# Optimization experiments

Measured on AMD Instinct MI355X. Metric: run time of the kernel, lower is better.

The kernel has to match this reference:

```python
import jax, jax.numpy as jnp
import numpy as np
from jax import lax

B, S = 64, 256            # batch, max_seq_len
EMB = 1024                # embed (== decoder_hidden, required by outs buffer)
ENC = 512                 # encoder_hidden; 2*ENC = 1024
DEC = 1024                # decoder_hidden
GIN = EMB + 2 * ENC       # GRUCell input size = 2048


def setup_inputs() -> dict:
    key = jax.random.key(0)
    ks = jax.random.split(key, 12)
    w = 0.02
    inp = {
        "input": jax.random.normal(ks[0], (B, S, EMB), jnp.float32),
        "hidden": jax.random.normal(ks[1], (DEC, B), jnp.float32),  # [decoder_hidden, batch]
        "encoder_outs": jax.random.normal(ks[2], (B, S, 2 * ENC), jnp.float32),
        "lengths": jnp.maximum(jax.random.randint(ks[3], (B,), 0, S), 1).astype(jnp.int32),
        # Attention params (additive / Bahdanau): v^T tanh(W_enc*enc + W_dec*h)
        "W_enc": jax.random.normal(ks[4], (2 * ENC, DEC), jnp.float32) * w,
        "W_dec": jax.random.normal(ks[5], (DEC, DEC), jnp.float32) * w,
        "v": jax.random.normal(ks[6], (DEC,), jnp.float32) * w,
        # GRUCell params (torch layout: W_ih [3H, GIN], W_hh [3H, H])
        "W_ih": jax.random.normal(ks[7], (3 * DEC, GIN), jnp.float32) * w,
        "W_hh": jax.random.normal(ks[8], (3 * DEC, DEC), jnp.float32) * w,
        "b_ih": jax.random.normal(ks[9], (3 * DEC,), jnp.float32) * w,
        "b_hh": jax.random.normal(ks[10], (3 * DEC,), jnp.float32) * w,
    }
    return inp


def reference(input, hidden, encoder_outs, lengths, W_enc, W_dec, v, W_ih, W_hh, b_ih, b_hh):
    h0 = hidden.T                                  # [B, DEC]
    mask = jnp.arange(S)[None, :] < lengths[:, None]   # [B, S]
    enc_proj = encoder_outs @ W_enc                # [B, S, DEC] (hoisted out of the loop)

    # One shared teacher-forcing coin flip per timestep (torch.rand(1) < 0.5),
    # made deterministic with a fixed key.
    tf_flags = jax.random.uniform(jax.random.key(1), (S - 1,)) < 0.5

    def attention(h):
        # energy: [B, S]
        energy = jnp.tanh(enc_proj + (h @ W_dec)[:, None, :]) @ v
        energy = jnp.where(mask, energy, jnp.float32(-1e9))
        attn = jax.nn.softmax(energy, axis=1)
        return jnp.einsum("bs,bse->be", attn, encoder_outs)  # [B, 2*ENC]

    def gru_cell(x, h):
        gi = x @ W_ih.T + b_ih                     # [B, 3*DEC]
        gh = h @ W_hh.T + b_hh
        i_r, i_z, i_n = jnp.split(gi, 3, axis=1)
        h_r, h_z, h_n = jnp.split(gh, 3, axis=1)
        r = jax.nn.sigmoid(i_r + h_r)
        z = jax.nn.sigmoid(i_z + h_z)
        n = jnp.tanh(i_n + r * h_n)
        return (1.0 - z) * n + z * h

    # teacher inputs for step t are input[:, t-1, :], t = 1..S-1
    teach_seq = jnp.swapaxes(input, 0, 1)[: S - 1]  # [S-1, B, EMB]

    def step(carry, xt):
        h, prev = carry
        teach, tf = xt
        ctx = attention(h)
        sel = jnp.where(tf, teach, prev)            # scalar bool broadcast
        h_new = gru_cell(jnp.concatenate([sel, ctx], axis=1), h)
        return (h_new, h_new), h_new

    (_, _), hs = lax.scan(step, (h0, input[:, 0, :]), (teach_seq, tf_flags))
    outs = jnp.concatenate([input[:, 0:1, :], jnp.swapaxes(hs, 0, 1)], axis=1)  # [B, S, DEC]
    return outs
```

## Files before the change

### kernel.cpp

```cpp
#include <hip/hip_runtime.h>
#include <stdint.h>

typedef unsigned short u16;
typedef unsigned int   u32;
typedef unsigned long long u64;
typedef __attribute__((ext_vector_type(8))) short short8;
typedef __attribute__((ext_vector_type(4))) short s16x4;
typedef __attribute__((ext_vector_type(4))) float f32x4;

#define MFMA(a,b,c) __builtin_amdgcn_mfma_f32_16x16x32_bf16((a),(b),(c),0,0,0)
#define NBLK 256
#define NTHR 256
#define SMEM_BYTES 160832

static const long kOutB = 256*1024;

__device__ __forceinline__ float b2f(u16 v){ union{u32 u; float f;} c; c.u = ((u32)v)<<16; return c.f; }
__device__ __forceinline__ u16 f2b(float f){ union{float f; u32 u;} c; c.f = f; u32 r = c.u + 0x7FFFu + ((c.u>>16)&1u); return (u16)(r>>16); }
__device__ __forceinline__ float fexp2(float x){ return __builtin_amdgcn_exp2f(x); }
__device__ __forceinline__ float frcp(float x){ return __builtin_amdgcn_rcpf(x); }
__device__ __forceinline__ float tanh_(float x){ float e = fexp2(x*2.885390081777927f); return 1.f - 2.f*frcp(e+1.f); }
__device__ __forceinline__ float sigm_(float x){ return frcp(1.f + fexp2(-1.4426950408889634f*x)); }

__device__ __forceinline__ u64 ald64(const void* p){
    return __hip_atomic_load((const u64*)p, __ATOMIC_RELAXED, __HIP_MEMORY_SCOPE_AGENT);
}
__device__ __forceinline__ u32 ald32(const void* p){
    return __hip_atomic_load((const u32*)p, __ATOMIC_RELAXED, __HIP_MEMORY_SCOPE_AGENT);
}
__device__ __forceinline__ void ast64(void* p, u64 v){
    __hip_atomic_store((u64*)p, v, __ATOMIC_RELAXED, __HIP_MEMORY_SCOPE_AGENT);
}
__device__ __forceinline__ void ast32(void* p, u32 v){
    __hip_atomic_store((u32*)p, v, __ATOMIC_RELAXED, __HIP_MEMORY_SCOPE_AGENT);
}

__device__ __forceinline__ u32 rotl32_(u32 x, int r){ return (x << r) | (x >> (32 - r)); }
__device__ bool tf_bit(u32 j){
    const u32 k0 = 0u, k1 = 1u, k2 = 0x1BD11BDAu ^ 0u ^ 1u;
    const int R0[4] = {13,15,26,6}, R1[4] = {17,29,16,24};
    u32 x0 = 0u, x1 = j;
    x0 += k0; x1 += k1;
    for(int i=0;i<4;i++){ x0 += x1; x1 = rotl32_(x1,R0[i]); x1 ^= x0; }
    x0 += k1; x1 += k2 + 1u;
    for(int i=0;i<4;i++){ x0 += x1; x1 = rotl32_(x1,R1[i]); x1 ^= x0; }
    x0 += k2; x1 += k0 + 2u;
    for(int i=0;i<4;i++){ x0 += x1; x1 = rotl32_(x1,R0[i]); x1 ^= x0; }
    x0 += k0; x1 += k1 + 3u;
    for(int i=0;i<4;i++){ x0 += x1; x1 = rotl32_(x1,R1[i]); x1 ^= x0; }
    x0 += k1; x1 += k2 + 4u;
    for(int i=0;i<4;i++){ x0 += x1; x1 = rotl32_(x1,R0[i]); x1 ^= x0; }
    x0 += k2; x1 += k0 + 5u;
    return (((x0 ^ x1) >> 31) == 0u);
}

__device__ __forceinline__ void gridbar(u32* sync){
    asm volatile("s_waitcnt vmcnt(0)" ::: "memory");
    __syncthreads();
    if(threadIdx.x == 0){
        u32* cnt  = sync;
        u32* gen  = sync + 32;
        u32* gcnt = sync + 64 + (blockIdx.x >> 5)*32;
        u32 g = __hip_atomic_load(gen, __ATOMIC_RELAXED, __HIP_MEMORY_SCOPE_AGENT);
        u32 a = __hip_atomic_fetch_add(gcnt, 1u, __ATOMIC_RELAXED, __HIP_MEMORY_SCOPE_AGENT);
        bool done = false;
        if(a == 31u){
            __hip_atomic_store(gcnt, 0u, __ATOMIC_RELAXED, __HIP_MEMORY_SCOPE_AGENT);
            asm volatile("s_waitcnt vmcnt(0)" ::: "memory");
            u32 b = __hip_atomic_fetch_add(cnt, 1u, __ATOMIC_RELAXED, __HIP_MEMORY_SCOPE_AGENT);
            if(b == 7u){
                __hip_atomic_store(cnt, 0u, __ATOMIC_RELAXED, __HIP_MEMORY_SCOPE_AGENT);
                asm volatile("s_waitcnt vmcnt(0)" ::: "memory");
                __hip_atomic_store(gen, g + 1u, __ATOMIC_RELAXED, __HIP_MEMORY_SCOPE_AGENT);
                done = true;
            }
        }
        if(!done)
            while(__hip_atomic_load(gen, __ATOMIC_RELAXED, __HIP_MEMORY_SCOPE_AGENT) == g)
                __builtin_amdgcn_s_sleep(1);
    }
    __syncthreads();
}

__global__ void k_cvt(const float* __restrict__ in, u16* __restrict__ out, int n){
    int i = blockIdx.x*blockDim.x + threadIdx.x;
    int st = gridDim.x*blockDim.x;
    for(; i < n; i += st) out[i] = f2b(in[i]);
}

__global__ void k_cvt_t(const float* __restrict__ in, u16* __restrict__ out, int R, int C){
    __shared__ float tile[32][33];
    int bx = blockIdx.x, by = blockIdx.y;
    int tx = threadIdx.x, ty = threadIdx.y;
    for(int j = 0; j < 32; j += 8) tile[ty+j][tx] = in[(by*32+ty+j)*C + bx*32+tx];
    __syncthreads();
    for(int j = 0; j < 32; j += 8) out[(bx*32+ty+j)*R + by*32+tx] = f2b(tile[tx][ty+j]);
}

__global__ void k_init(const float* __restrict__ hidden, const float* __restrict__ input,
                       float* __restrict__ h0f, u16* __restrict__ h0b, float* __restrict__ out,
                       u32* __restrict__ sync){
    int i = blockIdx.x*blockDim.x + threadIdx.x;
    int b = i >> 10, d = i & 1023;
    float h = hidden[d*64 + b];
    h0f[i] = h; h0b[i] = f2b(h);
    out[(long)b*kOutB + d] = input[(long)b*kOutB + d];
    if(i < 512) sync[i] = 0u;
}

__global__ __launch_bounds__(256) void k_gemm_ep(const u16* __restrict__ A, const u16* __restrict__ BT,
                                                 u16* __restrict__ Cb){
    int m0 = blockIdx.x*64, n0 = blockIdx.y*64;
    int w = threadIdx.x >> 6, l = threadIdx.x & 63;
    int r0 = l & 15, kh = (l >> 4) * 8;
    const u16* arow = A + (long)(m0 + w*16 + r0)*1024 + kh;
    f32x4 acc[4] = {};
    for(int k0 = 0; k0 < 1024; k0 += 32){
        short8 a = *(const short8*)(arow + k0);
        #pragma unroll
        for(int j = 0; j < 4; ++j){
            short8 b = *(const short8*)(BT + (long)(n0 + j*16 + r0)*1024 + k0 + kh);
            acc[j] = MFMA(a, b, acc[j]);
        }
    }
    int orow = m0 + w*16 + (l>>4)*4;
    int ocol = n0 + (l & 15);
    #pragma unroll
    for(int j = 0; j < 4; ++j)
        #pragma unroll
        for(int r = 0; r < 4; ++r)
            Cb[(long)(orow + r)*1024 + ocol + j*16] = f2b(acc[j][r]);
}

__global__ __launch_bounds__(NTHR, 1) void k_steps(
        const u16* __restrict__ epb, const float* __restrict__ input, const u16* __restrict__ encb,
        const u16* __restrict__ wihb, const u16* __restrict__ whhb, const u16* __restrict__ wdecT,
        const float* __restrict__ bih, const float* __restrict__ bhh,
        const float* __restrict__ vv, const int* __restrict__ lengths,
        float* __restrict__ hWrot, long hWstride,
        float* __restrict__ enyrot, long enystride,
        u16* __restrict__ crot, const float* __restrict__ hf0, u16* __restrict__ hrot,
        float* __restrict__ out, u32* __restrict__ sync){
    extern __shared__ char smem[];
    u16*   s_ep = (u16*)smem;
    float* sB   = (float*)(smem + 131072);
    float* sA   = (float*)(smem + 135168);
    float* sRed = (float*)(smem + 136192);
    f32x4* sAcc = (f32x4*)(smem + 136256);

    const int bid = blockIdx.x, tid = threadIdx.x;
    const int w = tid >> 6, l = tid & 63;
    const int r0 = l & 15, kh = (l >> 4) * 8;
    const int rg = bid >> 6, cg = bid & 63;
    const int p2_b = bid >> 2, p2_sq = bid & 3;
    const bool rotOn = (hWstride != 0);

    const int p2_len = lengths[p2_b];
    float rv[16];
    #pragma unroll
    for(int j = 0; j < 16; ++j) rv[j] = vv[l*16 + j];

    {
        const u16* src = epb + (long)(p2_b*256 + p2_sq*64)*1024;
        for(int i = tid; i < 8192; i += NTHR)
            *(short8*)(s_ep + i*8) = *(const short8*)(src + i*8);
    }
    __syncthreads();

    const u16* p1_brow = wdecT + (long)(cg*16 + r0)*1024 + w*256 + kh;
    const long p1_aoff = (long)(rg*16 + r0)*1024 + w*256 + kh;
    const int kxb = w*512, khb = w*256;
    const u16* b_wr = wihb + (long)(       cg*16 + r0)*2048 + kxb + kh;
    const u16* b_wz = wihb + (long)(1024 + cg*16 + r0)*2048 + kxb + kh;
    const u16* b_wn = wihb + (long)(2048 + cg*16 + r0)*2048 + kxb + kh;
    const u16* b_vr = whhb + (long)(       cg*16 + r0)*1024 + khb + kh;
    const u16* b_vz = whhb + (long)(1024 + cg*16 + r0)*1024 + khb + kh;
    const u16* b_vn = whhb + (long)(2048 + cg*16 + r0)*1024 + khb + kh;
    const long a_row_off = (long)(rg*16 + r0)*1024;
    const float* g_inf = input + (long)(rg*16 + r0)*kOutB;
    const int ucol = cg*16 + (l & 15);
    const float bir = bih[ucol], biz = bih[1024+ucol], bin_ = bih[2048+ucol];
    const float bhr = bhh[ucol], bhz = bhh[1024+ucol], bhn = bhh[2048+ucol];
    const int erow = rg*16 + (l>>4)*4;
    float hold[4];
    #pragma unroll
    for(int r = 0; r < 4; ++r) hold[r] = hf0[(erow + r)*1024 + ucol];

    for(int t = 1; t < 256; ++t){
        const u16* hbo = hrot + (size_t)(t-1)*65536;
        u16*       hbn = hrot + (size_t)t*65536;
        u16*       ctxt = crot + (size_t)(t-1)*65536;
        float*     hWt  = hWrot  + (size_t)(t-1)*hWstride;
        float*     enyt = enyrot + (size_t)(t-1)*enystride;
        {
            const u16* arow = hbo + p1_aoff;
            f32x4 acc = {};
            #pragma unroll
            for(int k0 = 0; k0 < 256; k0 += 32)
                acc = MFMA(*(const short8*)(arow + k0), *(const short8*)(p1_brow + k0), acc);
            sAcc[w*64 + l] = acc;
            __syncthreads();
            if(w == 0){
                f32x4 s = sAcc[l];
                s += sAcc[64 + l]; s += sAcc[128 + l]; s += sAcc[192 + l];
                #pragma unroll
                for(int r = 0; r < 4; ++r){
                    float mine = s[r];
                    float oth = __shfl_xor(mine, 1);
                    if(!(l & 1)){
                        union{ float f[2]; u64 q; } pk; pk.f[0] = mine; pk.f[1] = oth;
                        ast64(hWt + (erow + r)*1024 + cg*16 + (l & 15), pk.q);
                    }
                }
            }
        }
        gridbar(sync);
        {
            float rh[16];
            const float* hp = hWt + p2_b*1024 + l*16;
            if(rotOn){
                #pragma unroll
                for(int j4 = 0; j4 < 4; ++j4){
                    f32x4 v4 = *(const f32x4*)(hp + j4*4);
                    rh[j4*4+0] = v4.x; rh[j4*4+1] = v4.y;
                    rh[j4*4+2] = v4.z; rh[j4*4+3] = v4.w;
                }
            } else {
                #pragma unroll
                for(int j = 0; j < 8; ++j){
                    union{ u64 q; float f[2]; } uu; uu.q = ald64(hp + j*2);
                    rh[2*j] = uu.f[0]; rh[2*j+1] = uu.f[1];
                }
            }
            const u16* lrow = s_ep + (w*16)*1024 + l*16;
            for(int si = 0; si < 16; ++si){
                int s = p2_sq*64 + w*16 + si;
                short8 q0 = *(const short8*)(lrow + si*1024);
                short8 q1 = *(const short8*)(lrow + si*1024 + 8);
                float acc = 0.f;
                #pragma unroll
                for(int j = 0; j < 8; ++j) acc += rv[j]   * tanh_(b2f((u16)q0[j]) + rh[j]);
                #pragma unroll
                for(int j = 0; j < 8; ++j) acc += rv[8+j] * tanh_(b2f((u16)q1[j]) + rh[8+j]);
                #pragma unroll
                for(int off = 32; off; off >>= 1) acc += __shfl_xor(acc, off);
                if(l == 0){
                    float val = (s < p2_len) ? acc : -1e9f;
                    ast32(enyt + p2_b*256 + s, __float_as_uint(val));
                }
            }
        }
        gridbar(sync);
        {
            float e = rotOn ? enyt[p2_b*256 + tid]
                            : __uint_as_float(ald32(enyt + p2_b*256 + tid));
            float m = e;
            #pragma unroll
            for(int off = 32; off; off >>= 1) m = fmaxf(m, __shfl_xor(m, off));
            if(l == 0) sRed[w] = m;
            __syncthreads();
            m = fmaxf(fmaxf(sRed[0], sRed[1]), fmaxf(sRed[2], sRed[3]));
            float pp = fexp2((e - m)*1.4426950408889634f);
            sA[tid] = pp;
            float sm = pp;
            #pragma unroll
            for(int off = 32; off; off >>= 1) sm += __shfl_xor(sm, off);
            if(l == 0) sRed[4 + w] = sm;
            __syncthreads();
            float inv = 1.f / (sRed[4] + sRed[5] + sRed[6] + sRed[7]);
            const int half = l >> 5, cl = l & 31;
            const u16* ebase = encb + (long)p2_b*262144 + p2_sq*256 + cl*8;
            float acc[8] = {};
            #pragma unroll 8
            for(int i = 0; i < 32; ++i){
                int s = w*64 + i*2 + half;
                float ps = sA[s];
                short8 q = *(const short8*)(ebase + (long)s*1024);
                #pragma unroll
                for(int j = 0; j < 8; ++j) acc[j] += ps*b2f((u16)q[j]);
            }
            #pragma unroll
            for(int j = 0; j < 8; ++j) acc[j] += __shfl_xor(acc[j], 32);
            if(half == 0){
                #pragma unroll
                for(int j = 0; j < 8; ++j) sB[w*256 + cl*8 + j] = acc[j];
            }
            __syncthreads();
            float c = (sB[tid] + sB[256+tid] + sB[512+tid] + sB[768+tid]) * inv;
            u32 cb = (u32)f2b(c);
            u32 ob = (u32)__shfl_xor((int)cb, 1);
            if(!(tid & 1))
                ast32((u32*)ctxt + ((p2_b*1024 + p2_sq*256 + tid) >> 1), cb | (ob << 16));
        }
        gridbar(sync);
        {
            const bool useTeach = (t == 1) || tf_bit((u32)(t - 1));
            f32x4 a_r = {}, a_z = {}, a_n = {};
            if(w < 2){
                if(useTeach){
                    const float* sf = g_inf + (long)(t - 1)*1024 + kxb + kh;
                    for(int k0 = 0; k0 < 512; k0 += 32){
                        f32x4 u0q = *(const f32x4*)(sf + k0);
                        f32x4 u1q = *(const f32x4*)(sf + k0 + 4);
                        short8 a;
                        a[0]=(short)f2b(u0q.x); a[1]=(short)f2b(u0q.y);
                        a[2]=(short)f2b(u0q.z); a[3]=(short)f2b(u0q.w);
                        a[4]=(short)f2b(u1q.x); a[5]=(short)f2b(u1q.y);
                        a[6]=(short)f2b(u1q.z); a[7]=(short)f2b(u1q.w);
                        a_r = MFMA(a, *(const short8*)(b_wr + k0), a_r);
                        a_z = MFMA(a, *(const short8*)(b_wz + k0), a_z);
                        a_n = MFMA(a, *(const short8*)(b_wn + k0), a_n);
                    }
                } else {
                    const u16* ar = hbo + a_row_off + kxb + kh;
                    for(int k0 = 0; k0 < 512; k0 += 32){
                        short8 a = *(const short8*)(ar + k0);
                        a_r = MFMA(a, *(const short8*)(b_wr + k0), a_r);
                        a_z = MFMA(a, *(const short8*)(b_wz + k0), a_z);
                        a_n = MFMA(a, *(const short8*)(b_wn + k0), a_n);
                    }
                }
            } else {
                const u16* ar = ctxt + a_row_off + (kxb - 1024) + kh;
                for(int k0 = 0; k0 < 512; k0 += 32){
                    short8 a = *(const short8*)(ar + k0);
                    a_r = MFMA(a, *(const short8*)(b_wr + k0), a_r);
                    a_z = MFMA(a, *(const short8*)(b_wz + k0), a_z);
                    a_n = MFMA(a, *(const short8*)(b_wn + k0), a_n);
                }
            }
            f32x4 h_r = {}, h_z = {}, h_n = {};
            {
                const u16* ah = hbo + a_row_off + khb + kh;
                #pragma unroll
                for(int k0 = 0; k0 < 256; k0 += 32){
                    short8 h = *(const short8*)(ah + k0);
                    h_r = MFMA(h, *(const short8*)(b_vr + k0), h_r);
                    h_z = MFMA(h, *(const short8*)(b_vz + k0), h_z);
                    h_n = MFMA(h, *(const short8*)(b_vn + k0), h_n);
                }
            }
            sAcc[(w*6+0)*64 + l] = a_r;
            sAcc[(w*6+1)*64 + l] = a_z;
            sAcc[(w*6+2)*64 + l] = a_n;
            sAcc[(w*6+3)*64 + l] = h_r;
            sAcc[(w*6+4)*64 + l] = h_z;
            sAcc[(w*6+5)*64 + l] = h_n;
            __syncthreads();
            if(w == 0){
                f32x4 air = sAcc[0*64+l] + sAcc[6*64+l] + sAcc[12*64+l] + sAcc[18*64+l];
                f32x4 aiz = sAcc[1*64+l] + sAcc[7*64+l] + sAcc[13*64+l] + sAcc[19*64+l];
                f32x4 ain = sAcc[2*64+l] + sAcc[8*64+l] + sAcc[14*64+l] + sAcc[20*64+l];
                f32x4 ahr = sAcc[3*64+l] + sAcc[9*64+l] + sAcc[15*64+l] + sAcc[21*64+l];
                f32x4 ahz = sAcc[4*64+l] + sAcc[10*64+l] + sAcc[16*64+l] + sAcc[22*64+l];
                f32x4 ahn = sAcc[5*64+l] + sAcc[11*64+l] + sAcc[17*64+l] + sAcc[23*64+l];
                #pragma unroll
                for(int r = 0; r < 4; ++r){
                    int b = erow + r;
                    float rgt = sigm_(air[r] + bir + ahr[r] + bhr);
                    float z   = sigm_(aiz[r] + biz + ahz[r] + bhz);
                    float n   = tanh_(ain[r] + bin_ + rgt*(ahn[r] + bhn));
                    float hn = (1.f - z)*n + z*hold[r];
                    hold[r] = hn;
                    out[(long)b*kOutB + (long)t*1024 + ucol] = hn;
                    u32 mb = (u32)f2b(hn);
                    u32 ob = (u32)__shfl_xor((int)mb, 1);
                    if(!(l & 1))
                        ast32((u32*)hbn + ((b*1024 + ucol) >> 1), mb | (ob << 16));
                }
            }
        }
        gridbar(sync);
    }
}

extern "C" void kernel_launch(void* const* d_in, const int* in_sizes, int n_in,
                              void* d_out, int out_size, void* d_ws, size_t ws_size,
                              hipStream_t stream){
    (void)in_sizes; (void)n_in; (void)out_size;
    const float* input    = (const float*)d_in[0];
    const float* hidden   = (const float*)d_in[1];
    const float* enc_outs = (const float*)d_in[2];
    const int*   lengths  = (const int*)  d_in[3];
    const float* W_enc    = (const float*)d_in[4];
    const float* W_dec    = (const float*)d_in[5];
    const float* v        = (const float*)d_in[6];
    const float* W_ih     = (const float*)d_in[7];
    const float* W_hh     = (const float*)d_in[8];
    const float* b_ih     = (const float*)d_in[9];
    const float* b_hh     = (const float*)d_in[10];
    float* out = (float*)d_out;

    char* p = (char*)d_ws;
    auto alloc = [&](size_t bytes){ void* r = (void*)p; p += (bytes + 255) & ~(size_t)255; return r; };
    u16* epb   = (u16*)alloc((size_t)16384*1024*2);
    u16* encb  = (u16*)alloc((size_t)16384*1024*2);
    u16* wihb  = (u16*)alloc((size_t)3072*2048*2);
    u16* whhb  = (u16*)alloc((size_t)3072*1024*2);
    u16* wencT = (u16*)alloc((size_t)1024*1024*2);
    u16* wdecT = (u16*)alloc((size_t)1024*1024*2);
    float* hf0 = (float*)alloc((size_t)64*1024*4);
    u16* hrot  = (u16*)alloc((size_t)256*65536*2);
    u16* crot  = (u16*)alloc((size_t)255*65536*2);
    u32* sync  = (u32*)alloc(2048);
    size_t used = (size_t)(p - (char*)d_ws);
    size_t rotBytes = ((size_t)255*65536*4 + 256) + ((size_t)255*16384*4 + 256);
    long hWstride, enystride;
    float *hWrot, *enyrot;
    if(used + rotBytes <= ws_size){
        hWrot  = (float*)alloc((size_t)255*65536*4);
        enyrot = (float*)alloc((size_t)255*16384*4);
        hWstride = 65536; enystride = 16384;
    } else {
        hWrot  = (float*)alloc((size_t)65536*4);
        enyrot = (float*)alloc((size_t)16384*4);
        hWstride = 0; enystride = 0;
    }
    if((size_t)(p - (char*)d_ws) > ws_size) return;

    k_cvt<<<2048, 256, 0, stream>>>(enc_outs, encb, 16384*1024);
    k_cvt<<<1024, 256, 0, stream>>>(W_ih,     wihb, 3072*2048);
    k_cvt<<<512,  256, 0, stream>>>(W_hh,     whhb, 3072*1024);
    k_cvt_t<<<dim3(32,32), dim3(32,8), 0, stream>>>(W_enc, wencT, 1024, 1024);
    k_cvt_t<<<dim3(32,32), dim3(32,8), 0, stream>>>(W_dec, wdecT, 1024, 1024);
    k_init<<<256, 256, 0, stream>>>(hidden, input, hf0, hrot, out, sync);
    k_gemm_ep<<<dim3(256,16), 256, 0, stream>>>(encb, wencT, epb);

    hipFuncSetAttribute((const void*)k_steps, hipFuncAttributeMaxDynamicSharedMemorySize, SMEM_BYTES);
    k_steps<<<NBLK, NTHR, SMEM_BYTES, stream>>>(epb, input, encb, wihb, whhb, wdecT,
                                                b_ih, b_hh, v, lengths,
                                                hWrot, hWstride, enyrot, enystride,
                                                crot, hf0, hrot,
                                                out, sync);
}
```

Baseline: 10.25 ms.

## Replace grid barriers with per-group dataflow flags and store hW in bf16

```diff
diff --git a/kernel.cpp b/kernel.cpp
--- a/kernel.cpp
+++ b/kernel.cpp
@@ -82,6 +82,20 @@
     __syncthreads();
 }
 
+__device__ __forceinline__ void flag_signal(u32* f){
+    asm volatile("s_waitcnt vmcnt(0)" ::: "memory");
+    __syncthreads();
+    if(threadIdx.x == 0)
+        __hip_atomic_fetch_add(f, 1u, __ATOMIC_RELAXED, __HIP_MEMORY_SCOPE_AGENT);
+}
+__device__ __forceinline__ void flag_wait(u32* f, u32 target){
+    if(threadIdx.x == 0){
+        while(__hip_atomic_load(f, __ATOMIC_RELAXED, __HIP_MEMORY_SCOPE_AGENT) < target)
+            __builtin_amdgcn_s_sleep(1);
+    }
+    __syncthreads();
+}
+
 __global__ void k_cvt(const float* __restrict__ in, u16* __restrict__ out, int n){
     int i = blockIdx.x*blockDim.x + threadIdx.x;
     int st = gridDim.x*blockDim.x;
@@ -105,7 +119,7 @@
     float h = hidden[d*64 + b];
     h0f[i] = h; h0b[i] = f2b(h);
     out[(long)b*kOutB + d] = input[(long)b*kOutB + d];
-    if(i < 512) sync[i] = 0u;
+    if(i < 4096) sync[i] = 0u;
 }
 
 __global__ __launch_bounds__(256) void k_gemm_ep(const u16* __restrict__ A, const u16* __restrict__ BT,
@@ -137,7 +151,7 @@
         const u16* __restrict__ wihb, const u16* __restrict__ whhb, const u16* __restrict__ wdecT,
         const float* __restrict__ bih, const float* __restrict__ bhh,
         const float* __restrict__ vv, const int* __restrict__ lengths,
-        float* __restrict__ hWrot, long hWstride,
+        u16* __restrict__ hWrot, long hWstride,
         float* __restrict__ enyrot, long enystride,
         u16* __restrict__ crot, const float* __restrict__ hf0, u16* __restrict__ hrot,
         float* __restrict__ out, u32* __restrict__ sync){
@@ -153,7 +167,13 @@
     const int r0 = l & 15, kh = (l >> 4) * 8;
     const int rg = bid >> 6, cg = bid & 63;
     const int p2_b = bid >> 2, p2_sq = bid & 3;
-    const bool rotOn = (hWstride != 0);
+    const bool useFlags = (hWstride != 0);
+
+    u32* fbase = sync + 1024;
+    u32* f_h = fbase +        rg*32;
+    u32* f_w = fbase + 128  + rg*32;
+    u32* f_c = fbase + 256  + rg*32;
+    u32* f_e = fbase + 512  + p2_b*32;
 
     const int p2_len = lengths[p2_b];
     float rv[16];
@@ -190,8 +210,9 @@
         const u16* hbo = hrot + (size_t)(t-1)*65536;
         u16*       hbn = hrot + (size_t)t*65536;
         u16*       ctxt = crot + (size_t)(t-1)*65536;
-        float*     hWt  = hWrot  + (size_t)(t-1)*hWstride;
+        u16*       hWt  = hWrot  + (size_t)(t-1)*hWstride;
         float*     enyt = enyrot + (size_t)(t-1)*enystride;
+        if(useFlags) flag_wait(f_h, 64u*(u32)(t-1));
         {
             const u16* arow = hbo + p1_aoff;
             f32x4 acc = {};
@@ -205,31 +226,29 @@
                 s += sAcc[64 + l]; s += sAcc[128 + l]; s += sAcc[192 + l];
                 #pragma unroll
                 for(int r = 0; r < 4; ++r){
-                    float mine = s[r];
-                    float oth = __shfl_xor(mine, 1);
-                    if(!(l & 1)){
-                        union{ float f[2]; u64 q; } pk; pk.f[0] = mine; pk.f[1] = oth;
-                        ast64(hWt + (erow + r)*1024 + cg*16 + (l & 15), pk.q);
-                    }
-                }
-            }
-        }
-        gridbar(sync);
+                    u32 mb = (u32)f2b(s[r]);
+                    u32 ob = (u32)__shfl_xor((int)mb, 1);
+                    if(!(l & 1))
+                        ast32((u32*)hWt + (((erow + r)*1024 + cg*16 + (l & 15)) >> 1), mb | (ob << 16));
+                }
+            }
+        }
+        if(useFlags) flag_signal(f_w); else gridbar(sync);
+        if(useFlags) flag_wait(f_w, 64u*(u32)t);
         {
             float rh[16];
-            const float* hp = hWt + p2_b*1024 + l*16;
-            if(rotOn){
+            const u16* hp = hWt + p2_b*1024 + l*16;
+            if(useFlags){
+                short8 h0 = *(const short8*)(hp);
+                short8 h1 = *(const short8*)(hp + 8);
+                #pragma unroll
+                for(int j = 0; j < 8; ++j){ rh[j] = b2f((u16)h0[j]); rh[8+j] = b2f((u16)h1[j]); }
+            } else {
                 #pragma unroll
                 for(int j4 = 0; j4 < 4; ++j4){
-                    f32x4 v4 = *(const f32x4*)(hp + j4*4);
-                    rh[j4*4+0] = v4.x; rh[j4*4+1] = v4.y;
-                    rh[j4*4+2] = v4.z; rh[j4*4+3] = v4.w;
-                }
-            } else {
-                #pragma unroll
-                for(int j = 0; j < 8; ++j){
-                    union{ u64 q; float f[2]; } uu; uu.q = ald64(hp + j*2);
-                    rh[2*j] = uu.f[0]; rh[2*j+1] = uu.f[1];
+                    u64 q = ald64(hp + j4*4);
+                    rh[j4*4+0] = b2f((u16)(q      )); rh[j4*4+1] = b2f((u16)(q >> 16));
+                    rh[j4*4+2] = b2f((u16)(q >> 32)); rh[j4*4+3] = b2f((u16)(q >> 48));
                 }
             }
             const u16* lrow = s_ep + (w*16)*1024 + l*16;
@@ -250,10 +269,11 @@
                 }
             }
         }
-        gridbar(sync);
+        if(useFlags) flag_signal(f_e); else gridbar(sync);
+        if(useFlags) flag_wait(f_e, 4u*(u32)t);
         {
-            float e = rotOn ? enyt[p2_b*256 + tid]
-                            : __uint_as_float(ald32(enyt + p2_b*256 + tid));
+            float e = useFlags ? enyt[p2_b*256 + tid]
+                               : __uint_as_float(ald32(enyt + p2_b*256 + tid));
             float m = e;
             #pragma unroll
             for(int off = 32; off; off >>= 1) m = fmaxf(m, __shfl_xor(m, off));
@@ -292,7 +312,8 @@
             if(!(tid & 1))
                 ast32((u32*)ctxt + ((p2_b*1024 + p2_sq*256 + tid) >> 1), cb | (ob << 16));
         }
-        gridbar(sync);
+        if(useFlags) flag_signal(f_c); else gridbar(sync);
+        if(useFlags) flag_wait(f_c, 64u*(u32)t);
         {
             const bool useTeach = (t == 1) || tf_bit((u32)(t - 1));
             f32x4 a_r = {}, a_z = {}, a_n = {};
@@ -370,7 +391,7 @@
                 }
             }
         }
-        gridbar(sync);
+        if(useFlags) flag_signal(f_h); else gridbar(sync);
     }
 }
 
@@ -402,17 +423,17 @@
     float* hf0 = (float*)alloc((size_t)64*1024*4);
     u16* hrot  = (u16*)alloc((size_t)256*65536*2);
     u16* crot  = (u16*)alloc((size_t)255*65536*2);
-    u32* sync  = (u32*)alloc(2048);
+    u32* sync  = (u32*)alloc(16384);
     size_t used = (size_t)(p - (char*)d_ws);
-    size_t rotBytes = ((size_t)255*65536*4 + 256) + ((size_t)255*16384*4 + 256);
+    size_t rotBytes = ((size_t)255*65536*2 + 256) + ((size_t)255*16384*4 + 256);
     long hWstride, enystride;
-    float *hWrot, *enyrot;
+    u16 *hWrot; float *enyrot;
     if(used + rotBytes <= ws_size){
-        hWrot  = (float*)alloc((size_t)255*65536*4);
+        hWrot  = (u16*)  alloc((size_t)255*65536*2);
         enyrot = (float*)alloc((size_t)255*16384*4);
         hWstride = 65536; enystride = 16384;
     } else {
-        hWrot  = (float*)alloc((size_t)65536*4);
+        hWrot  = (u16*)  alloc((size_t)65536*2);
         enyrot = (float*)alloc((size_t)16384*4);
         hWstride = 0; enystride = 0;
     }
```

Result: no change. 10.23 ms (-0.2%).
